# Optimization experiments

Measured on AMD Instinct MI355X. Metric: run time of the kernel, lower is better.

The kernel has to match this reference:

```python
import jax, jax.numpy as jnp
import numpy as np

N_NODES = 50000
N_EDGES = 800000
IN_FEATS = 128
OUT_FEATS = 128


def mean_agg(feat, src, dst, num_nodes):
    # DGL copy_u + mean reduce: mean of in-neighbor (src) features per dst node;
    # nodes with zero in-degree get 0.
    msg = feat[src]                                        # [E, D] gather
    summed = jax.ops.segment_sum(msg, dst, num_segments=num_nodes)  # [N, D]
    deg = jax.ops.segment_sum(jnp.ones((src.shape[0],), feat.dtype), dst,
                              num_segments=num_nodes)      # [N]
    return summed / jnp.maximum(deg, 1.0)[:, None]


def setup_inputs() -> dict:
    key = jax.random.key(0)
    ks = jax.random.split(key, 16)
    sx = 1.0 / np.sqrt(IN_FEATS)
    sh = 1.0 / np.sqrt(OUT_FEATS)
    inp = {
        "x": jax.random.normal(ks[0], (N_NODES, IN_FEATS), jnp.float32),
        "h": jax.random.normal(ks[1], (N_NODES, OUT_FEATS), jnp.float32),
        "c": jax.random.normal(ks[2], (N_NODES, OUT_FEATS), jnp.float32),
        # stacked weights for the 4 gates (order: i, f, c, o)
        "Wx_self": jax.random.normal(ks[3], (4, IN_FEATS, OUT_FEATS), jnp.float32) * sx,
        "Wx_neigh": jax.random.normal(ks[4], (4, IN_FEATS, OUT_FEATS), jnp.float32) * sx,
        "Wh_self": jax.random.normal(ks[5], (4, OUT_FEATS, OUT_FEATS), jnp.float32) * sh,
        "Wh_neigh": jax.random.normal(ks[6], (4, OUT_FEATS, OUT_FEATS), jnp.float32) * sh,
        "w_ci": jax.random.uniform(ks[7], (OUT_FEATS,), jnp.float32),
        "w_cf": jax.random.uniform(ks[8], (OUT_FEATS,), jnp.float32),
        "w_co": jax.random.uniform(ks[9], (OUT_FEATS,), jnp.float32),
        "b_i": jax.random.uniform(ks[10], (OUT_FEATS,), jnp.float32),
        "b_f": jax.random.uniform(ks[11], (OUT_FEATS,), jnp.float32),
        "b_c": jax.random.uniform(ks[12], (OUT_FEATS,), jnp.float32),
        "b_o": jax.random.uniform(ks[13], (OUT_FEATS,), jnp.float32),
        "src": jax.random.randint(ks[14], (N_EDGES,), 0, N_NODES, jnp.int32),
        "dst": jax.random.randint(ks[15], (N_EDGES,), 0, N_NODES, jnp.int32),
    }
    return inp


def reference(x, h, c, Wx_self, Wx_neigh, Wh_self, Wh_neigh,
              w_ci, w_cf, w_co, b_i, b_f, b_c, b_o, src, dst):
    n = x.shape[0]
    # reuse_gate_rz=True: compute the two mean-aggregations once, shared by all nets
    h_N = mean_agg(x, src, dst, n)      # neighbor mean of x  [N, in]
    h_agg = mean_agg(h, src, dst, n)    # neighbor mean of h  [N, out]

    # each sub-net: net(g, feat, h_N=agg) = feat @ W_self + agg @ W_neigh
    # batched over the 4 gates (i, f, c, o)
    gx = jnp.einsum('ni,gio->gno', x, Wx_self) + jnp.einsum('ni,gio->gno', h_N, Wx_neigh)
    gh = jnp.einsum('no,goe->gne', h, Wh_self) + jnp.einsum('no,goe->gne', h_agg, Wh_neigh)
    s = gx + gh                          # [4, N, out]

    i = jax.nn.sigmoid(s[0] + w_ci * c + b_i)
    f = jax.nn.sigmoid(s[1] + w_cf * c + b_f)
    c_tilde = jnp.tanh(s[2] + b_c)
    new_c = f * c + i * c_tilde
    o = jax.nn.sigmoid(s[3] + w_co * new_c + b_o)
    new_h = o * jnp.tanh(new_c)
    return new_h, new_c
```

## Files before the change

### kernel.cpp

```cpp
#include <hip/hip_runtime.h>
#include <hip/hip_bf16.h>
#include <stdint.h>

#define N_NODES 50000
#define N_EDGES 800000
#define D 128
#define NPAD 50048
#define HKD 256
#define KDIM 512

typedef __attribute__((ext_vector_type(8))) __bf16 bf16x8;
typedef __attribute__((ext_vector_type(4))) __bf16 bf16x4;
typedef __attribute__((ext_vector_type(4))) float f32x4;
typedef __attribute__((ext_vector_type(2))) float f32x2;

__device__ __forceinline__ void gload_lds16(const void* g, void* l) {
  __builtin_amdgcn_global_load_lds(
      (const __attribute__((address_space(1))) unsigned int*)(uintptr_t)g,
      (__attribute__((address_space(3))) unsigned int*)(uint32_t)(uintptr_t)l,
      16, 0, 0);
}

__device__ __forceinline__ float sigm(float v) { return 1.0f / (1.0f + __expf(-v)); }
__device__ __forceinline__ float tanh_fast(float v) { return 1.0f - 2.0f / (1.0f + __expf(2.0f * v)); }

#if defined(__has_builtin) && __has_builtin(__builtin_amdgcn_cvt_pk_fp8_f32) && __has_builtin(__builtin_amdgcn_cvt_pk_f32_fp8)
__device__ __forceinline__ unsigned pack_fp8x4(float a, float b, float c, float d) {
  int p = __builtin_amdgcn_cvt_pk_fp8_f32(a, b, 0, false);
  p = __builtin_amdgcn_cvt_pk_fp8_f32(c, d, p, true);
  return (unsigned)p;
}
__device__ __forceinline__ f32x2 unpk_fp8_lo(unsigned u) { return __builtin_amdgcn_cvt_pk_f32_fp8(u, false); }
__device__ __forceinline__ f32x2 unpk_fp8_hi(unsigned u) { return __builtin_amdgcn_cvt_pk_f32_fp8(u, true); }
#else
#include <hip/hip_fp8.h>
__device__ __forceinline__ unsigned pack_fp8x4(float a, float b, float c, float d) {
  __hip_fp8_e4m3 qa(a), qb(b), qc(c), qd(d);
  return (unsigned)qa.__x | ((unsigned)qb.__x << 8) | ((unsigned)qc.__x << 16) | ((unsigned)qd.__x << 24);
}
__device__ __forceinline__ float unpk1(unsigned byte) {
  __hip_fp8_e4m3 t; t.__x = (__hip_fp8_storage_t)byte; return (float)t;
}
__device__ __forceinline__ f32x2 unpk_fp8_lo(unsigned u) { f32x2 r; r.x = unpk1(u & 0xff); r.y = unpk1((u >> 8) & 0xff); return r; }
__device__ __forceinline__ f32x2 unpk_fp8_hi(unsigned u) { f32x2 r; r.x = unpk1((u >> 16) & 0xff); r.y = unpk1(u >> 24); return r; }
#endif

#define NB_DEG 3125
#define NB_TOB 6250
#define NB_PKW 1024
__global__ void k_pre(const int* __restrict__ dst, int* __restrict__ deg,
                      const float* __restrict__ x, const float* __restrict__ h,
                      __bf16* __restrict__ XHb, uint8_t* __restrict__ XH8,
                      const float* __restrict__ Wx_self, const float* __restrict__ Wx_neigh,
                      const float* __restrict__ Wh_self, const float* __restrict__ Wh_neigh,
                      __bf16* __restrict__ Wp) {
  int b = blockIdx.x;
  if (b < NB_DEG) {
    int e = b * 256 + threadIdx.x;
    atomicAdd(&deg[dst[e]], 1);
  } else if (b < NB_DEG + NB_TOB) {
    int idx = (b - NB_DEG) * 256 + threadIdx.x;
    int node = idx >> 5;
    int f4 = (idx & 31) << 2;
    float4 xv = *(const float4*)(x + (size_t)node * D + f4);
    float4 hv = *(const float4*)(h + (size_t)node * D + f4);
    bf16x4 a, bb;
    a[0] = (__bf16)xv.x; a[1] = (__bf16)xv.y; a[2] = (__bf16)xv.z; a[3] = (__bf16)xv.w;
    bb[0] = (__bf16)hv.x; bb[1] = (__bf16)hv.y; bb[2] = (__bf16)hv.z; bb[3] = (__bf16)hv.w;
    __bf16* br = XHb + (size_t)node * HKD;
    *(bf16x4*)(br + f4) = a;
    *(bf16x4*)(br + 128 + f4) = bb;
    uint8_t* r8 = XH8 + (size_t)node * HKD;
    *(unsigned*)(r8 + f4) = pack_fp8x4(xv.x, xv.y, xv.z, xv.w);
    *(unsigned*)(r8 + 128 + f4) = pack_fp8x4(hv.x, hv.y, hv.z, hv.w);
  } else {
    int idx = (b - NB_DEG - NB_TOB) * 256 + threadIdx.x;
    int e = idx & 7;
    int r16 = (idx >> 3) & 15;
    int q = (idx >> 7) & 3;
    int s = (idx >> 9) & 15;
    int G = idx >> 13;
    int wrow = G * 16 + r16;
    int g = wrow >> 7, o = wrow & 127;
    int k = s * 32 + q * 8 + e;
    const float* src; int i;
    if (k < 128)      { src = Wx_self;  i = k; }
    else if (k < 256) { src = Wh_self;  i = k - 128; }
    else if (k < 384) { src = Wx_neigh; i = k - 256; }
    else              { src = Wh_neigh; i = k - 384; }
    Wp[idx] = (__bf16)src[(g << 14) + (i << 7) + o];
  }
}

__global__ __launch_bounds__(1024) void k_scan(const int* __restrict__ deg, int* __restrict__ offs,
                                               int* __restrict__ cursor, int n) {
  const int t = threadIdx.x;
  const int lane = t & 63;
  const int w = t >> 6;
  __shared__ int wsum[16];
  __shared__ int carry_s;
  int carry = 0;
  for (int base = 0; base < n; base += 4096) {
    int idx = base + t * 4;
    int4 v = make_int4(0, 0, 0, 0);
    if (idx < n) v = *(const int4*)(deg + idx);
    int tsum = v.x + v.y + v.z + v.w;
    int s = tsum;
#pragma unroll
    for (int d = 1; d < 64; d <<= 1) {
      int u = __shfl_up(s, d, 64);
      if (lane >= d) s += u;
    }
    if (lane == 63) wsum[w] = s;
    __syncthreads();
    int woff = 0;
    for (int i = 0; i < w; i++) woff += wsum[i];
    int excl = carry + woff + (s - tsum);
    if (idx < n) {
      int4 o;
      o.x = excl; o.y = excl + v.x; o.z = o.y + v.y; o.w = o.z + v.z;
      *(int4*)(offs + idx) = o;
      *(int4*)(cursor + idx) = o;
    }
    __syncthreads();
    if (t == 0) {
      int tot = carry;
#pragma unroll
      for (int i = 0; i < 16; i++) tot += wsum[i];
      carry_s = tot;
    }
    __syncthreads();
    carry = carry_s;
  }
  if (t == 0) offs[n] = carry;
}

__global__ void k_fill(const int* __restrict__ src, const int* __restrict__ dst,
                       int* __restrict__ cursor, int* __restrict__ bins) {
  int e = blockIdx.x * 256 + threadIdx.x;
  if (e < N_EDGES) {
    int d = dst[e];
    int p = atomicAdd(&cursor[d], 1);
    bins[p] = src[e];
  }
}

__global__ void k_gather(const int* __restrict__ offs, const int* __restrict__ bins,
                         const uint8_t* __restrict__ XH8, uint8_t* __restrict__ ZM8) {
  int wid = (blockIdx.x * 256 + threadIdx.x) >> 6;
  int lane = threadIdx.x & 63;
  if (wid >= N_NODES) return;
  const int half = lane >> 5;
  const int li = lane & 31;
  const int boff = li * 8;
  int beg = offs[wid], end = offs[wid + 1];
  float a[8] = {0.f, 0.f, 0.f, 0.f, 0.f, 0.f, 0.f, 0.f};
  auto acc = [&](uint2 v) {
    f32x2 p;
    p = unpk_fp8_lo(v.x); a[0] += p.x; a[1] += p.y;
    p = unpk_fp8_hi(v.x); a[2] += p.x; a[3] += p.y;
    p = unpk_fp8_lo(v.y); a[4] += p.x; a[5] += p.y;
    p = unpk_fp8_hi(v.y); a[6] += p.x; a[7] += p.y;
  };
  int j = beg + half;
  for (; j + 6 < end; j += 8) {
    int s0 = bins[j], s1 = bins[j + 2], s2 = bins[j + 4], s3 = bins[j + 6];
    uint2 v0 = *(const uint2*)(XH8 + (size_t)s0 * HKD + boff);
    uint2 v1 = *(const uint2*)(XH8 + (size_t)s1 * HKD + boff);
    uint2 v2 = *(const uint2*)(XH8 + (size_t)s2 * HKD + boff);
    uint2 v3 = *(const uint2*)(XH8 + (size_t)s3 * HKD + boff);
    acc(v0); acc(v1); acc(v2); acc(v3);
  }
  for (; j < end; j += 2) {
    uint2 v = *(const uint2*)(XH8 + (size_t)bins[j] * HKD + boff);
    acc(v);
  }
#pragma unroll
  for (int e = 0; e < 8; ++e) a[e] += __shfl_xor(a[e], 32, 64);
  int degn = end - beg;
  float inv = 1.0f / (float)(degn > 0 ? degn : 1);
  if (lane < 32) {
    unsigned lo = pack_fp8x4(a[0] * inv, a[1] * inv, a[2] * inv, a[3] * inv);
    unsigned hi = pack_fp8x4(a[4] * inv, a[5] * inv, a[6] * inv, a[7] * inv);
    *(uint2*)(ZM8 + (size_t)wid * HKD + boff) = make_uint2(lo, hi);
  }
}

__global__ __launch_bounds__(512, 4) void k_gemm(
    const __bf16* __restrict__ XHb, const uint8_t* __restrict__ ZM8, const __bf16* __restrict__ Wp,
    const float* __restrict__ c,
    const float* __restrict__ w_ci, const float* __restrict__ w_cf, const float* __restrict__ w_co,
    const float* __restrict__ b_i, const float* __restrict__ b_f, const float* __restrict__ b_c,
    const float* __restrict__ b_o,
    float* __restrict__ out_h, float* __restrict__ out_c) {
  __shared__ __align__(16) __bf16 As[4096 * 8];
  const int t = threadIdx.x;
  const int lane = t & 63;
  const int w = t >> 6;
  const int m0 = blockIdx.x * 64;
  const int l15 = lane & 15;
  const int q = lane >> 4;

#pragma unroll
  for (int i = 0; i < 4; ++i) {
    int u = i * 512 + t;
    int row = u >> 5, cz = u & 31;
    int cg = cz ^ (row & 7);
    int grow = m0 + row;
    if (grow >= N_NODES) grow = N_NODES - 1;
    gload_lds16(XHb + (size_t)grow * HKD + cg * 8, (__bf16*)As + (size_t)u * 8);
  }
#pragma unroll
  for (int i = 0; i < 4; ++i) {
    int u = i * 512 + t;
    int row = u >> 5, cz = u & 31;
    int grow = m0 + row;
    if (grow >= N_NODES) grow = N_NODES - 1;
    uint2 v = *(const uint2*)(ZM8 + (size_t)grow * HKD + cz * 8);
    bf16x8 bb;
    f32x2 p;
    p = unpk_fp8_lo(v.x); bb[0] = (__bf16)p.x; bb[1] = (__bf16)p.y;
    p = unpk_fp8_hi(v.x); bb[2] = (__bf16)p.x; bb[3] = (__bf16)p.y;
    p = unpk_fp8_lo(v.y); bb[4] = (__bf16)p.x; bb[5] = (__bf16)p.y;
    p = unpk_fp8_hi(v.y); bb[6] = (__bf16)p.x; bb[7] = (__bf16)p.y;
    int slot = 2048 + row * 32 + (cz ^ (row & 7));
    *(bf16x8*)((__bf16*)As + (size_t)slot * 8) = bb;
  }
  __syncthreads();

  f32x4 acc[4][4];
#pragma unroll
  for (int m = 0; m < 4; ++m)
#pragma unroll
    for (int g = 0; g < 4; ++g) acc[m][g] = (f32x4){0.f, 0.f, 0.f, 0.f};

  auto LOADA = [&](int step, bf16x8* af) {
    const int base = (step < 8) ? 0 : 2048;
    const int cq = ((step < 8) ? step : (step - 8)) * 4 + q;
#pragma unroll
    for (int m = 0; m < 4; ++m) {
      int row = m * 16 + l15;
      af[m] = *(const bf16x8*)((__bf16*)As + (size_t)(base + row * 32 + (cq ^ (row & 7))) * 8);
    }
  };

  const __bf16* wp = Wp + (size_t)(w * 16) * 512 + lane * 8;

  bf16x8 bA[4], bB[4];
#pragma unroll
  for (int g = 0; g < 4; ++g) bA[g] = *(const bf16x8*)(wp + g * 65536);

#pragma unroll
  for (int s2 = 0; s2 < 8; ++s2) {
    {
      const int step = 2 * s2;
#pragma unroll
      for (int g = 0; g < 4; ++g)
        bB[g] = *(const bf16x8*)(wp + g * 65536 + (step + 1) * 512);
      bf16x8 af[4];
      LOADA(step, af);
      __builtin_amdgcn_s_setprio(1);
#pragma unroll
      for (int m = 0; m < 4; ++m)
#pragma unroll
        for (int g = 0; g < 4; ++g)
          acc[m][g] = __builtin_amdgcn_mfma_f32_16x16x32_bf16(af[m], bA[g], acc[m][g], 0, 0, 0);
      __builtin_amdgcn_s_setprio(0);
    }
    {
      const int step = 2 * s2 + 1;
      if (step < 15) {
#pragma unroll
        for (int g = 0; g < 4; ++g)
          bA[g] = *(const bf16x8*)(wp + g * 65536 + (step + 1) * 512);
      }
      bf16x8 af[4];
      LOADA(step, af);
      __builtin_amdgcn_s_setprio(1);
#pragma unroll
      for (int m = 0; m < 4; ++m)
#pragma unroll
        for (int g = 0; g < 4; ++g)
          acc[m][g] = __builtin_amdgcn_mfma_f32_16x16x32_bf16(af[m], bB[g], acc[m][g], 0, 0, 0);
      __builtin_amdgcn_s_setprio(0);
    }
  }

  const int o = w * 16 + l15;
  const float wci = w_ci[o], wcf = w_cf[o], wco = w_co[o];
  const float bi = b_i[o], bfv = b_f[o], bc = b_c[o], bo = b_o[o];
#pragma unroll
  for (int m = 0; m < 4; ++m) {
#pragma unroll
    for (int r = 0; r < 4; ++r) {
      int row = m0 + m * 16 + q * 4 + r;
      if (row < N_NODES) {
        float cv = c[(size_t)row * D + o];
        float ig = sigm(acc[m][0][r] + wci * cv + bi);
        float fg = sigm(acc[m][1][r] + wcf * cv + bfv);
        float ct = tanh_fast(acc[m][2][r] + bc);
        float nc = fg * cv + ig * ct;
        float og = sigm(acc[m][3][r] + wco * nc + bo);
        out_h[(size_t)row * D + o] = og * tanh_fast(nc);
        out_c[(size_t)row * D + o] = nc;
      }
    }
  }
}

extern "C" void kernel_launch(void* const* d_in, const int* in_sizes, int n_in,
                              void* d_out, int out_size, void* d_ws, size_t ws_size,
                              hipStream_t stream) {
  const float* x = (const float*)d_in[0];
  const float* h = (const float*)d_in[1];
  const float* c = (const float*)d_in[2];
  const float* Wx_self = (const float*)d_in[3];
  const float* Wx_neigh = (const float*)d_in[4];
  const float* Wh_self = (const float*)d_in[5];
  const float* Wh_neigh = (const float*)d_in[6];
  const float* w_ci = (const float*)d_in[7];
  const float* w_cf = (const float*)d_in[8];
  const float* w_co = (const float*)d_in[9];
  const float* b_i = (const float*)d_in[10];
  const float* b_f = (const float*)d_in[11];
  const float* b_c = (const float*)d_in[12];
  const float* b_o = (const float*)d_in[13];
  const int* src = (const int*)d_in[14];
  const int* dst = (const int*)d_in[15];

  char* ws = (char*)d_ws;
  int* deg = (int*)(ws);
  int* offs = (int*)(ws + 200704);
  int* cursor = (int*)(ws + 400896);
  int* bins = (int*)(ws + 601088);
  uint8_t* XH8 = (uint8_t*)(ws + 4194304);
  uint8_t* ZM8 = (uint8_t*)(ws + 17039360);
  __bf16* Wp = (__bf16*)(ws + 29884416);

  float* out_h = (float*)d_out;
  float* out_c = out_h + (size_t)N_NODES * D;
  __bf16* XHb = (__bf16*)out_h;

  hipMemsetAsync(deg, 0, N_NODES * sizeof(int), stream);
  k_pre<<<NB_DEG + NB_TOB + NB_PKW, 256, 0, stream>>>(dst, deg, x, h, XHb, XH8,
                                                      Wx_self, Wx_neigh, Wh_self, Wh_neigh, Wp);
  k_scan<<<1, 1024, 0, stream>>>(deg, offs, cursor, N_NODES);
  k_fill<<<(N_EDGES + 255) / 256, 256, 0, stream>>>(src, dst, cursor, bins);
  k_gather<<<(N_NODES + 3) / 4, 256, 0, stream>>>(offs, bins, XH8, ZM8);
  k_gemm<<<NPAD / 64, 512, 0, stream>>>(XHb, ZM8, Wp, c, w_ci, w_cf, w_co,
                                        b_i, b_f, b_c, b_o, out_h, out_c);
}
```

Baseline: 217.2 us.

## Store neighbor means as bf16 in output buffer and DMA them into LDS

The gather kernel now writes the neighbor-mean activations as bf16 into the not-yet-written out_c buffer instead of as fp8 in workspace. The GEMM kernel can then copy them straight into LDS with async global-to-LDS loads, replacing the register unpack-and-store path. Its K loop is split into two halves with explicit waitcnt and barriers, meant to overlap the copy with the first half of the MFMA work. The scan kernel also handles 8 degrees per thread instead of 4, halving its loop iterations. The price is twice the bytes for the mean buffer on both the write and the read side, but precision improves over fp8.

```diff
diff --git a/kernel.cpp b/kernel.cpp
--- a/kernel.cpp
+++ b/kernel.cpp
@@ -100,11 +100,14 @@
   __shared__ int wsum[16];
   __shared__ int carry_s;
   int carry = 0;
-  for (int base = 0; base < n; base += 4096) {
-    int idx = base + t * 4;
-    int4 v = make_int4(0, 0, 0, 0);
-    if (idx < n) v = *(const int4*)(deg + idx);
-    int tsum = v.x + v.y + v.z + v.w;
+  for (int base = 0; base < n; base += 8192) {
+    int idx = base + t * 8;
+    int4 v0 = make_int4(0, 0, 0, 0), v1 = make_int4(0, 0, 0, 0);
+    if (idx < n) {
+      v0 = *(const int4*)(deg + idx);
+      v1 = *(const int4*)(deg + idx + 4);
+    }
+    int tsum = v0.x + v0.y + v0.z + v0.w + v1.x + v1.y + v1.z + v1.w;
     int s = tsum;
 #pragma unroll
     for (int d = 1; d < 64; d <<= 1) {
@@ -117,10 +120,11 @@
     for (int i = 0; i < w; i++) woff += wsum[i];
     int excl = carry + woff + (s - tsum);
     if (idx < n) {
-      int4 o;
-      o.x = excl; o.y = excl + v.x; o.z = o.y + v.y; o.w = o.z + v.z;
-      *(int4*)(offs + idx) = o;
-      *(int4*)(cursor + idx) = o;
+      int4 o0, o1;
+      o0.x = excl;        o0.y = o0.x + v0.x; o0.z = o0.y + v0.y; o0.w = o0.z + v0.z;
+      o1.x = o0.w + v0.w; o1.y = o1.x + v1.x; o1.z = o1.y + v1.y; o1.w = o1.z + v1.z;
+      *(int4*)(offs + idx) = o0;     *(int4*)(offs + idx + 4) = o1;
+      *(int4*)(cursor + idx) = o0;   *(int4*)(cursor + idx + 4) = o1;
     }
     __syncthreads();
     if (t == 0) {
@@ -146,7 +150,7 @@
 }
 
 __global__ void k_gather(const int* __restrict__ offs, const int* __restrict__ bins,
-                         const uint8_t* __restrict__ XH8, uint8_t* __restrict__ ZM8) {
+                         const uint8_t* __restrict__ XH8, __bf16* __restrict__ ZM) {
   int wid = (blockIdx.x * 256 + threadIdx.x) >> 6;
   int lane = threadIdx.x & 63;
   if (wid >= N_NODES) return;
@@ -180,14 +184,15 @@
   int degn = end - beg;
   float inv = 1.0f / (float)(degn > 0 ? degn : 1);
   if (lane < 32) {
-    unsigned lo = pack_fp8x4(a[0] * inv, a[1] * inv, a[2] * inv, a[3] * inv);
-    unsigned hi = pack_fp8x4(a[4] * inv, a[5] * inv, a[6] * inv, a[7] * inv);
-    *(uint2*)(ZM8 + (size_t)wid * HKD + boff) = make_uint2(lo, hi);
+    bf16x8 bb;
+#pragma unroll
+    for (int e = 0; e < 8; ++e) bb[e] = (__bf16)(a[e] * inv);
+    *(bf16x8*)(ZM + (size_t)wid * HKD + boff) = bb;
   }
 }
 
 __global__ __launch_bounds__(512, 4) void k_gemm(
-    const __bf16* __restrict__ XHb, const uint8_t* __restrict__ ZM8, const __bf16* __restrict__ Wp,
+    const __bf16* __restrict__ XHb, const __bf16* __restrict__ ZM, const __bf16* __restrict__ Wp,
     const float* __restrict__ c,
     const float* __restrict__ w_ci, const float* __restrict__ w_cf, const float* __restrict__ w_co,
     const float* __restrict__ b_i, const float* __restrict__ b_f, const float* __restrict__ b_c,
@@ -214,19 +219,11 @@
   for (int i = 0; i < 4; ++i) {
     int u = i * 512 + t;
     int row = u >> 5, cz = u & 31;
+    int cg = cz ^ (row & 7);
     int grow = m0 + row;
     if (grow >= N_NODES) grow = N_NODES - 1;
-    uint2 v = *(const uint2*)(ZM8 + (size_t)grow * HKD + cz * 8);
-    bf16x8 bb;
-    f32x2 p;
-    p = unpk_fp8_lo(v.x); bb[0] = (__bf16)p.x; bb[1] = (__bf16)p.y;
-    p = unpk_fp8_hi(v.x); bb[2] = (__bf16)p.x; bb[3] = (__bf16)p.y;
-    p = unpk_fp8_lo(v.y); bb[4] = (__bf16)p.x; bb[5] = (__bf16)p.y;
-    p = unpk_fp8_hi(v.y); bb[6] = (__bf16)p.x; bb[7] = (__bf16)p.y;
-    int slot = 2048 + row * 32 + (cz ^ (row & 7));
-    *(bf16x8*)((__bf16*)As + (size_t)slot * 8) = bb;
-  }
-  __syncthreads();
+    gload_lds16(ZM + (size_t)grow * HKD + cg * 8, (__bf16*)As + (size_t)(2048 + u) * 8);
+  }
 
   f32x4 acc[4][4];
 #pragma unroll
@@ -245,13 +242,52 @@
   };
 
   const __bf16* wp = Wp + (size_t)(w * 16) * 512 + lane * 8;
-
   bf16x8 bA[4], bB[4];
 #pragma unroll
   for (int g = 0; g < 4; ++g) bA[g] = *(const bf16x8*)(wp + g * 65536);
 
-#pragma unroll
-  for (int s2 = 0; s2 < 8; ++s2) {
+  asm volatile("s_waitcnt vmcnt(4)" ::: "memory");
+  __builtin_amdgcn_s_barrier();
+  __builtin_amdgcn_sched_barrier(0);
+#pragma unroll
+  for (int s2 = 0; s2 < 4; ++s2) {
+    {
+      const int step = 2 * s2;
+#pragma unroll
+      for (int g = 0; g < 4; ++g)
+        bB[g] = *(const bf16x8*)(wp + g * 65536 + (step + 1) * 512);
+      bf16x8 af[4];
+      LOADA(step, af);
+      __builtin_amdgcn_s_setprio(1);
+#pragma unroll
+      for (int m = 0; m < 4; ++m)
+#pragma unroll
+        for (int g = 0; g < 4; ++g)
+          acc[m][g] = __builtin_amdgcn_mfma_f32_16x16x32_bf16(af[m], bA[g], acc[m][g], 0, 0, 0);
+      __builtin_amdgcn_s_setprio(0);
+    }
+    {
+      const int step = 2 * s2 + 1;
+#pragma unroll
+      for (int g = 0; g < 4; ++g)
+        bA[g] = *(const bf16x8*)(wp + g * 65536 + (step + 1) * 512);
+      bf16x8 af[4];
+      LOADA(step, af);
+      __builtin_amdgcn_s_setprio(1);
+#pragma unroll
+      for (int m = 0; m < 4; ++m)
+#pragma unroll
+        for (int g = 0; g < 4; ++g)
+          acc[m][g] = __builtin_amdgcn_mfma_f32_16x16x32_bf16(af[m], bB[g], acc[m][g], 0, 0, 0);
+      __builtin_amdgcn_s_setprio(0);
+    }
+  }
+
+  asm volatile("s_waitcnt vmcnt(0)" ::: "memory");
+  __builtin_amdgcn_s_barrier();
+  __builtin_amdgcn_sched_barrier(0);
+#pragma unroll
+  for (int s2 = 4; s2 < 8; ++s2) {
     {
       const int step = 2 * s2;
 #pragma unroll
@@ -334,19 +370,19 @@
   int* cursor = (int*)(ws + 400896);
   int* bins = (int*)(ws + 601088);
   uint8_t* XH8 = (uint8_t*)(ws + 4194304);
-  uint8_t* ZM8 = (uint8_t*)(ws + 17039360);
-  __bf16* Wp = (__bf16*)(ws + 29884416);
+  __bf16* Wp = (__bf16*)(ws + 17039360);
 
   float* out_h = (float*)d_out;
   float* out_c = out_h + (size_t)N_NODES * D;
   __bf16* XHb = (__bf16*)out_h;
+  __bf16* ZM = (__bf16*)out_c;
 
   hipMemsetAsync(deg, 0, N_NODES * sizeof(int), stream);
   k_pre<<<NB_DEG + NB_TOB + NB_PKW, 256, 0, stream>>>(dst, deg, x, h, XHb, XH8,
                                                       Wx_self, Wx_neigh, Wh_self, Wh_neigh, Wp);
   k_scan<<<1, 1024, 0, stream>>>(deg, offs, cursor, N_NODES);
   k_fill<<<(N_EDGES + 255) / 256, 256, 0, stream>>>(src, dst, cursor, bins);
-  k_gather<<<(N_NODES + 3) / 4, 256, 0, stream>>>(offs, bins, XH8, ZM8);
-  k_gemm<<<NPAD / 64, 512, 0, stream>>>(XHb, ZM8, Wp, c, w_ci, w_cf, w_co,
+  k_gather<<<(N_NODES + 3) / 4, 256, 0, stream>>>(offs, bins, XH8, ZM);
+  k_gemm<<<NPAD / 64, 512, 0, stream>>>(XHb, ZM, Wp, c, w_ci, w_cf, w_co,
                                         b_i, b_f, b_c, b_o, out_h, out_c);
 }
```

Result: faster. 208.5 us (-4.0%).
